# Performance work log

Measured on AMD Instinct MI355X. Metric: run time of the kernel, lower is better.

Reference implementation:

```python
import jax, jax.numpy as jnp
import numpy as np

N_NODE, N_USER, N_PRICE, EMB = 100000, 40000, 100, 128
E_VV, E_VP, E_VU, E_UV = 2000000, 200000, 2000000, 2000000


def _spmm(rows, cols, vals, x, n_rows):
    # sparse COO (n_rows, n_cols) @ x  -> (n_rows, d)
    return jax.ops.segment_sum(vals[:, None] * x[cols], rows, num_segments=n_rows)


def _row_norm_spmm(rows, cols, vals, x, n_rows):
    # torch.sparse.mm followed by division by row-sum of values (+1e-8)
    num = _spmm(rows, cols, vals, x, n_rows)
    den = jax.ops.segment_sum(vals, rows, num_segments=n_rows)[:, None] + 1e-8
    return num / den


def _linear(x, W, b):
    return x @ W.T + b


def setup_inputs() -> dict:
    key = jax.random.key(0)
    ks = jax.random.split(key, 40)
    d = {}
    d['embedding'] = jax.random.normal(ks[0], (N_NODE, EMB), jnp.float32) * 0.1
    d['pri_emb'] = jax.random.normal(ks[1], (N_PRICE, EMB), jnp.float32) * 0.1
    d['user_emb'] = jax.random.normal(ks[2], (N_USER, EMB), jnp.float32) * 0.1
    d['adj_rows'] = jax.random.randint(ks[3], (E_VV,), 0, N_NODE, jnp.int32)
    d['adj_cols'] = jax.random.randint(ks[4], (E_VV,), 0, N_NODE, jnp.int32)
    d['adj_vals'] = jax.random.uniform(ks[5], (E_VV,), jnp.float32)
    d['vp_rows'] = jax.random.randint(ks[6], (E_VP,), 0, N_NODE, jnp.int32)
    d['vp_cols'] = jax.random.randint(ks[7], (E_VP,), 0, N_PRICE, jnp.int32)
    d['vp_vals'] = jax.random.uniform(ks[8], (E_VP,), jnp.float32)
    d['vu_rows'] = jax.random.randint(ks[9], (E_VU,), 0, N_NODE, jnp.int32)
    d['vu_cols'] = jax.random.randint(ks[10], (E_VU,), 0, N_USER, jnp.int32)
    d['vu_vals'] = jax.random.uniform(ks[11], (E_VU,), jnp.float32)
    d['pv_rows'] = jax.random.randint(ks[12], (E_VP,), 0, N_PRICE, jnp.int32)
    d['pv_cols'] = jax.random.randint(ks[13], (E_VP,), 0, N_NODE, jnp.int32)
    d['pv_vals'] = jax.random.uniform(ks[14], (E_VP,), jnp.float32)
    d['uv_rows'] = jax.random.randint(ks[15], (E_UV,), 0, N_USER, jnp.int32)
    d['uv_cols'] = jax.random.randint(ks[16], (E_UV,), 0, N_NODE, jnp.int32)
    d['uv_vals'] = jax.random.uniform(ks[17], (E_UV,), jnp.float32)
    d['item_price_indices'] = jax.random.randint(ks[18], (N_NODE,), 0, N_PRICE, jnp.int32)
    s = 0.02
    d['mat_vu'] = jax.random.normal(ks[19], (N_NODE, 1), jnp.float32) * s
    d['mat_pv'] = jax.random.normal(ks[20], (N_PRICE, 1), jnp.float32) * s
    d['mat_uv'] = jax.random.normal(ks[21], (N_USER, 1), jnp.float32) * s
    d['W_aogi'] = jax.random.normal(ks[22], (EMB, 2 * EMB), jnp.float32) * s
    d['b_aogi'] = jnp.zeros((EMB,), jnp.float32)
    d['W_bgi1'] = jax.random.normal(ks[23], (EMB, EMB), jnp.float32) * s
    d['b_bgi1'] = jnp.zeros((EMB,), jnp.float32)
    d['W_aogp'] = jax.random.normal(ks[24], (EMB, 2 * EMB), jnp.float32) * s
    d['b_aogp'] = jnp.zeros((EMB,), jnp.float32)
    d['W_bgp1'] = jax.random.normal(ks[25], (EMB, EMB), jnp.float32) * s
    d['b_bgp1'] = jnp.zeros((EMB,), jnp.float32)
    d['W_user'] = jax.random.normal(ks[26], (EMB, 3 * EMB), jnp.float32) * s
    d['b_user'] = jnp.zeros((EMB,), jnp.float32)
    d['user_lambda'] = jnp.asarray(0.2, jnp.float32)
    return d


def _forward(embedding, pri_emb, user_emb,
             adj_rows, adj_cols, adj_vals,
             vp_rows, vp_cols, vp_vals,
             vu_rows, vu_cols, vu_vals,
             pv_rows, pv_cols, pv_vals,
             uv_rows, uv_cols, uv_vals,
             item_price_indices,
             mat_vu, mat_pv, mat_uv,
             W_aogi, b_aogi, W_bgi1, b_bgi1,
             W_aogp, b_aogp, W_bgp1, b_bgp1,
             W_user, b_user, user_lambda,
             layers=1):
    def inter_gate(Wa, ba, Wb, bb, e1, e2):
        gate = jax.nn.sigmoid(_linear(jnp.concatenate([e1, e2], 1), Wa, ba) + _linear(e1, Wb, bb))
        return e1 + gate * e2  # dropout50 = identity at eval

    def intra_gate(rows, cols, vals, mat_v, emb2, n_rows):
        # torch version computes the chunked row-normalized spmm under no_grad
        alpha = jax.lax.stop_gradient(_row_norm_spmm(rows, cols, vals, emb2, n_rows))
        return alpha * mat_v  # dropout70 = identity at eval

    for _ in range(layers):
        item = (inter_gate(W_aogi, b_aogi, W_bgi1, b_bgi1, embedding,
                           _spmm(vp_rows, vp_cols, vp_vals, pri_emb, N_NODE))
                + _spmm(adj_rows, adj_cols, adj_vals, embedding, N_NODE)
                + user_lambda * intra_gate(vu_rows, vu_cols, vu_vals, mat_vu, user_emb, N_NODE))
        price = inter_gate(W_aogp, b_aogp, W_bgp1, b_bgp1, pri_emb,
                           intra_gate(pv_rows, pv_cols, pv_vals, mat_pv, embedding, N_PRICE))
        e_price_user = _spmm(uv_rows, uv_cols, uv_vals, pri_emb[item_price_indices], N_USER)
        e_item_user = intra_gate(uv_rows, uv_cols, uv_vals, mat_uv, embedding, N_USER)
        gate = jax.nn.sigmoid(_linear(jnp.concatenate([user_emb, e_item_user, e_price_user], -1), W_user, b_user))
        user = gate * user_emb + (1.0 - gate) * e_item_user
        embedding, pri_emb, user_emb = item, price, user
    return item, price, user


def reference(embedding, pri_emb, user_emb,
              adj_rows, adj_cols, adj_vals,
              vp_rows, vp_cols, vp_vals,
              vu_rows, vu_cols, vu_vals,
              pv_rows, pv_cols, pv_vals,
              uv_rows, uv_cols, uv_vals,
              item_price_indices,
              mat_vu, mat_pv, mat_uv,
              W_aogi, b_aogi, W_bgi1, b_bgi1,
              W_aogp, b_aogp, W_bgp1, b_bgp1,
              W_user, b_user, user_lambda):
    return _forward(embedding, pri_emb, user_emb,
                    adj_rows, adj_cols, adj_vals,
                    vp_rows, vp_cols, vp_vals,
                    vu_rows, vu_cols, vu_vals,
                    pv_rows, pv_cols, pv_vals,
                    uv_rows, uv_cols, uv_vals,
                    item_price_indices,
                    mat_vu, mat_pv, mat_uv,
                    W_aogi, b_aogi, W_bgi1, b_bgi1,
                    W_aogp, b_aogp, W_bgp1, b_bgp1,
                    W_user, b_user, user_lambda)
```

## Files before the change

kernel.cpp:

```cpp
#include <hip/hip_runtime.h>
#include <hip/hip_bf16.h>

#define N_NODE 100000
#define N_USER 40000
#define N_PRICE 100
#define EMB 128
#define E_VV 2000000
#define E_VP 200000
#define E_VU 2000000
#define E_UV 2000000

#define FOFF0 0
#define FOFF1 256
#define FOFF2 512
#define FOFF3 767
#define FOFF4 1023
#define FTOT  1073
#define EPB   8192
#define BK1 245
#define BK2 490
#define BK3 735
#define BK4 760
#define BKT 785
#define CB1 256
#define CB2 512
#define CB3 767
#define CB4 1023
#define CBT 1073
#define RB_PV   100
#define RB_ITEM 25000
#define RB_USER 10000
#define RBT (RB_PV + RB_ITEM + RB_USER)
#define FB_ITEM 782
#define FB_USER 313
#define FBT (FB_ITEM + FB_USER + 50)

typedef __attribute__((ext_vector_type(8))) short short8;
typedef __attribute__((ext_vector_type(4))) float f32x4;

__device__ __forceinline__ float sigf(float x){ return 1.f/(1.f+__expf(-x)); }
__device__ __forceinline__ unsigned bfr(float f){
  unsigned u = __float_as_uint(f);
  return (u + 0x7FFFu + ((u>>16)&1u)) >> 16;
}
__device__ __forceinline__ float bf_lo(unsigned u){ return __uint_as_float(u << 16); }
__device__ __forceinline__ float bf_hi(unsigned u){ return __uint_as_float(u & 0xFFFF0000u); }
__device__ __forceinline__ unsigned pack2(float x, float y){ return bfr(x) | (bfr(y)<<16); }

__global__ __launch_bounds__(256) void k_cvt_all(
    const float4* __restrict__ se, const float4* __restrict__ su, const float4* __restrict__ sp,
    uint2* __restrict__ de, uint2* __restrict__ du, uint2* __restrict__ dp){
  const int nE = N_NODE*EMB/4, nU = N_USER*EMB/4, nP = N_PRICE*EMB/4;
  int i = blockIdx.x*256 + threadIdx.x;
  const float4* src; uint2* dst; int j;
  if (i < nE){ src = se; dst = de; j = i; }
  else if (i < nE+nU){ src = su; dst = du; j = i-nE; }
  else if (i < nE+nU+nP){ src = sp; dst = dp; j = i-nE-nU; }
  else return;
  float4 v = src[j];
  dst[j] = make_uint2(bfr(v.x) | (bfr(v.y)<<16), bfr(v.z) | (bfr(v.w)<<16));
}

__global__ __launch_bounds__(256) void k_prep(
    const float* __restrict__ Wa, const float* __restrict__ Wb, const float* __restrict__ Wu,
    ushort* __restrict__ Wc, ushort* __restrict__ Wub,
    int* __restrict__ fill,
    int2* __restrict__ adjE, int2* __restrict__ vuE, int2* __restrict__ uvE,
    int2* __restrict__ vpE, int2* __restrict__ pvE){
  if (blockIdx.x == 320){
    int t = threadIdx.x;
    for (int i = t; i < FTOT; i += 256) fill[i] = 0;
    if (t < 16){
      int2 z = make_int2(0,0);
      adjE[E_VV+t] = z; vuE[E_VU+t] = z; uvE[E_UV+t] = z; vpE[E_VP+t] = z; pvE[E_VP+t] = z;
    }
    return;
  }
  int idx = blockIdx.x*256 + threadIdx.x;
  if (idx < 128*256){
    int n = idx >> 8, k = idx & 255;
    float v = Wa[n*256+k] + ((k < 128) ? Wb[n*128+k] : 0.f);
    Wc[idx] = (ushort)bfr(v);
  } else {
    int j = idx - 128*256;
    if (j < 128*384) Wub[j] = (ushort)bfr(Wu[j]);
  }
}

template<int E, int RPB, int NB, int CAPc>
__device__ __forceinline__ void bucket_body(int blk,
    const int* __restrict__ rows, const int* __restrict__ cols, const float* __restrict__ vals,
    int* __restrict__ fill, uint2* __restrict__ stg,
    int* cnt, int* gbase, int* lbase, uint2* stage)
{
  const int t = threadIdx.x;
  const int e0 = blk * EPB;
  for (int i = t; i < NB; i += 256) cnt[i] = 0;
  __syncthreads();
  #pragma unroll 4
  for (int i = 0; i < 32; ++i){
    int e = e0 + i*256 + t;
    if (e < E) atomicAdd(&cnt[rows[e]/RPB], 1);
  }
  __syncthreads();
  if (t < 64){
    int run = 0;
    for (int c0 = 0; c0 < NB; c0 += 64){
      int j = c0 + t;
      int x = (j < NB) ? cnt[j] : 0;
      int s = x;
      #pragma unroll
      for (int d = 1; d < 64; d <<= 1){ int y = __shfl_up(s, d); if (t >= d) s += y; }
      if (j < NB) lbase[j] = run + s - x;
      run += __shfl(s, 63);
    }
  }
  __syncthreads();
  for (int b = t; b < NB; b += 256){
    int c = cnt[b];
    gbase[b] = (c > 0) ? atomicAdd(&fill[b], c) : 0;
    cnt[b] = lbase[b];
  }
  __syncthreads();
  #pragma unroll 4
  for (int i = 0; i < 32; ++i){
    int e = e0 + i*256 + t;
    if (e < E){
      int r = rows[e];
      int b = r/RPB, rl = r - b*RPB;
      int pos = atomicAdd(&cnt[b], 1);
      stage[pos] = make_uint2((unsigned)cols[e] | ((unsigned)rl << 17), __float_as_uint(vals[e]));
    }
  }
  __syncthreads();
  const int wid = t >> 6, lane = t & 63;
  for (int b = wid; b < NB; b += 4){
    int lb = lbase[b];
    int n = cnt[b] - lb;
    int gb = gbase[b];
    for (int j = lane; j < n; j += 64){
      int slot = gb + j; if (slot >= CAPc) slot = CAPc - 1;
      stg[(size_t)b*CAPc + slot] = stage[lb + j];
    }
  }
}

__global__ __launch_bounds__(256) void k_bucket_all(
    const int* __restrict__ aR, const int* __restrict__ aC, const float* __restrict__ aV,
    const int* __restrict__ uR, const int* __restrict__ uC, const float* __restrict__ uV,
    const int* __restrict__ vR, const int* __restrict__ vC, const float* __restrict__ vV,
    const int* __restrict__ pR, const int* __restrict__ pC, const float* __restrict__ pV,
    const int* __restrict__ qR, const int* __restrict__ qC, const float* __restrict__ qV,
    int* __restrict__ fill,
    uint2* __restrict__ stgA, uint2* __restrict__ stgU, uint2* __restrict__ stgV,
    uint2* __restrict__ stgP, uint2* __restrict__ stgQ)
{
  __shared__ int cnt[256], gbase[256], lbase[256];
  __shared__ uint2 stage[EPB];
  int b = blockIdx.x;
  if      (b < BK1) bucket_body<E_VV,391,256,8704>(b,      aR,aC,aV, fill+FOFF0, stgA, cnt, gbase, lbase, stage);
  else if (b < BK2) bucket_body<E_VU,391,256,8704>(b-BK1,  uR,uC,uV, fill+FOFF1, stgU, cnt, gbase, lbase, stage);
  else if (b < BK3) bucket_body<E_UV,157,255,8704>(b-BK2,  vR,vC,vV, fill+FOFF2, stgV, cnt, gbase, lbase, stage);
  else if (b < BK4) bucket_body<E_VP,391,256,1536>(b-BK3,  pR,pC,pV, fill+FOFF3, stgP, cnt, gbase, lbase, stage);
  else              bucket_body<E_VP,  2, 50,5120>(b-BK4,  qR,qC,qV, fill+FOFF4, stgQ, cnt, gbase, lbase, stage);
}

template<int NROW, int RPB, int NB, int CAPc>
__device__ __forceinline__ void csr_body(int b,
    const uint2* __restrict__ stg, const int* __restrict__ fill,
    int* __restrict__ start, int2* __restrict__ csr,
    int* cnt, uint2* stage, int* sbase)
{
  const int t = threadIdx.x;
  const int row0 = b * RPB;
  int R = NROW - row0; if (R > RPB) R = RPB;
  int count = fill[b]; if (count > CAPc) count = CAPc;
  for (int i = t; i < R; i += 256) cnt[i] = 0;
  if (t < 64){
    int run = 0;
    for (int c0 = 0; c0 < NB; c0 += 64){
      int j = c0 + t;
      int x = (j < NB) ? fill[j] : 0;
      int s = x;
      #pragma unroll
      for (int d = 1; d < 64; d <<= 1){ int y = __shfl_up(s, d); if (t >= d) s += y; }
      if (j == b) *sbase = run + s - x;
      run += __shfl(s, 63);
    }
  }
  __syncthreads();
  const int base = *sbase;
  const uint2* mystg = stg + (size_t)b*CAPc;
  for (int j = t; j < count; j += 256)
    atomicAdd(&cnt[mystg[j].x >> 17], 1);
  __syncthreads();
  if (t < 64){
    int run = 0;
    for (int c0 = 0; c0 < R; c0 += 64){
      int i = c0 + t;
      int x = (i < R) ? cnt[i] : 0;
      int s = x;
      #pragma unroll
      for (int d = 1; d < 64; d <<= 1){ int y = __shfl_up(s, d); if (t >= d) s += y; }
      if (i < R) cnt[i] = run + s - x;
      run += __shfl(s, 63);
    }
  }
  __syncthreads();
  for (int i = t; i < R; i += 256) start[row0 + i] = base + cnt[i];
  if (b == NB-1 && t == 0) start[NROW] = base + count;
  __syncthreads();
  for (int j = t; j < count; j += 256){
    uint2 kv = mystg[j];
    int rl = kv.x >> 17;
    int pos = atomicAdd(&cnt[rl], 1);
    stage[pos] = kv;
  }
  __syncthreads();
  for (int j = t; j < count; j += 256){
    uint2 kv = stage[j];
    csr[base + j] = make_int2((int)(kv.x & 0x1FFFF), (int)kv.y);
  }
}

__global__ __launch_bounds__(256) void k_csr_all(
    const uint2* __restrict__ stgA, const uint2* __restrict__ stgU, const uint2* __restrict__ stgV,
    const uint2* __restrict__ stgP, const uint2* __restrict__ stgQ,
    const int* __restrict__ fill,
    int* __restrict__ aS, int* __restrict__ uS, int* __restrict__ vS,
    int* __restrict__ pS, int* __restrict__ qS,
    int2* __restrict__ aE, int2* __restrict__ uE, int2* __restrict__ vE,
    int2* __restrict__ pE, int2* __restrict__ qE)
{
  __shared__ int cnt[391];
  __shared__ int sbase;
  __shared__ uint2 stage[8704];
  int b = blockIdx.x;
  if      (b < CB1) csr_body<N_NODE,391,256,8704>(b,     stgA, fill+FOFF0, aS, aE, cnt, stage, &sbase);
  else if (b < CB2) csr_body<N_NODE,391,256,8704>(b-CB1, stgU, fill+FOFF1, uS, uE, cnt, stage, &sbase);
  else if (b < CB3) csr_body<N_USER,157,255,8704>(b-CB2, stgV, fill+FOFF2, vS, vE, cnt, stage, &sbase);
  else if (b < CB4) csr_body<N_NODE,391,256,1536>(b-CB3, stgP, fill+FOFF3, pS, pE, cnt, stage, &sbase);
  else              csr_body<N_PRICE,  2, 50,5120>(b-CB4, stgQ, fill+FOFF4, qS, qE, cnt, stage, &sbase);
}


#define FMA8(ACC, U, V)                                     \
  ACC[0] += (V)*bf_lo((U).x); ACC[1] += (V)*bf_hi((U).x);   \
  ACC[2] += (V)*bf_lo((U).y); ACC[3] += (V)*bf_hi((U).y);   \
  ACC[4] += (V)*bf_lo((U).z); ACC[5] += (V)*bf_hi((U).z);   \
  ACC[6] += (V)*bf_lo((U).w); ACC[7] += (V)*bf_hi((U).w);

#define RED8(ACC)                                           \
  _Pragma("unroll")                                         \
  for (int j = 0; j < 8; ++j){                              \
    ACC[j] += __shfl_xor(ACC[j], 16);                       \
    ACC[j] += __shfl_xor(ACC[j], 32);                       \
  }

__device__ __forceinline__ void item_body(int rb,
    const uint4* __restrict__ be4, const uint4* __restrict__ bu4, const uint4* __restrict__ bp4,
    const int* __restrict__ aS, const int2* __restrict__ aE,
    const int* __restrict__ uS, const int2* __restrict__ uE,
    const int* __restrict__ pS, const int2* __restrict__ pE,
    const float* __restrict__ mat_vu, const float* __restrict__ lam,
    float4* __restrict__ out4, uint4* __restrict__ vp4)
{
  const int r = rb*4 + (threadIdx.x >> 6);
  const int l = threadIdx.x & 63;
  const int g = l >> 4, q = l & 15;
  float aA[8] = {}, aU[8] = {}, aP[8] = {};
  float den = 0.f;
  int s = aS[r], e = aS[r+1];
  for (int i = s; i < e; i += 16){
    int2 cv[4]; uint4 u[4];
    #pragma unroll
    for (int k = 0; k < 4; ++k) cv[k] = aE[i + 4*k + g];
    #pragma unroll
    for (int k = 0; k < 4; ++k) u[k] = be4[(size_t)cv[k].x*16 + q];
    #pragma unroll
    for (int k = 0; k < 4; ++k){
      float v = (i + 4*k + g < e) ? __int_as_float(cv[k].y) : 0.f;
      FMA8(aA, u[k], v)
    }
  }
  s = uS[r]; e = uS[r+1];
  for (int i = s; i < e; i += 16){
    int2 cv[4]; uint4 u[4];
    #pragma unroll
    for (int k = 0; k < 4; ++k) cv[k] = uE[i + 4*k + g];
    #pragma unroll
    for (int k = 0; k < 4; ++k) u[k] = bu4[(size_t)cv[k].x*16 + q];
    #pragma unroll
    for (int k = 0; k < 4; ++k){
      float v = (i + 4*k + g < e) ? __int_as_float(cv[k].y) : 0.f;
      FMA8(aU, u[k], v)
      den += v;
    }
  }
  s = pS[r]; e = pS[r+1];
  for (int i = s; i < e; i += 16){
    int2 cv[4]; uint4 u[4];
    #pragma unroll
    for (int k = 0; k < 4; ++k) cv[k] = pE[i + 4*k + g];
    #pragma unroll
    for (int k = 0; k < 4; ++k) u[k] = bp4[(size_t)cv[k].x*16 + q];
    #pragma unroll
    for (int k = 0; k < 4; ++k){
      float v = (i + 4*k + g < e) ? __int_as_float(cv[k].y) : 0.f;
      FMA8(aP, u[k], v)
    }
  }
  RED8(aA) RED8(aU) RED8(aP)
  den += __shfl_xor(den, 16); den += __shfl_xor(den, 32);
  float sc = lam[0]*mat_vu[r]/(den + 1e-8f);
  if (g == 0){
    out4[(size_t)r*32 + q*2]     = make_float4(aA[0]+sc*aU[0], aA[1]+sc*aU[1], aA[2]+sc*aU[2], aA[3]+sc*aU[3]);
    out4[(size_t)r*32 + q*2 + 1] = make_float4(aA[4]+sc*aU[4], aA[5]+sc*aU[5], aA[6]+sc*aU[6], aA[7]+sc*aU[7]);
    vp4[(size_t)r*16 + q] = make_uint4(pack2(aP[0],aP[1]), pack2(aP[2],aP[3]), pack2(aP[4],aP[5]), pack2(aP[6],aP[7]));
  }
}

__device__ __forceinline__ void user_body(int rb,
    const uint4* __restrict__ be4, const uint4* __restrict__ bp4,
    const int* __restrict__ S, const int2* __restrict__ E,
    const int* __restrict__ ipi, const float* __restrict__ mat_uv,
    uint4* __restrict__ eit4, uint4* __restrict__ uvp4)
{
  const int r = rb*4 + (threadIdx.x >> 6);
  const int l = threadIdx.x & 63;
  const int g = l >> 4, q = l & 15;
  float aI[8] = {}, aP[8] = {};
  float den = 0.f;
  int s = S[r], e = S[r+1];
  for (int i = s; i < e; i += 8){
    int2 cv[2];
    #pragma unroll
    for (int k = 0; k < 2; ++k) cv[k] = E[i + 4*k + g];
    uint4 u[2]; int ip[2];
    #pragma unroll
    for (int k = 0; k < 2; ++k){ u[k] = be4[(size_t)cv[k].x*16 + q]; ip[k] = ipi[cv[k].x]; }
    uint4 y[2];
    #pragma unroll
    for (int k = 0; k < 2; ++k) y[k] = bp4[(size_t)ip[k]*16 + q];
    #pragma unroll
    for (int k = 0; k < 2; ++k){
      float v = (i + 4*k + g < e) ? __int_as_float(cv[k].y) : 0.f;
      FMA8(aI, u[k], v)
      FMA8(aP, y[k], v)
      den += v;
    }
  }
  RED8(aI) RED8(aP)
  den += __shfl_xor(den, 16); den += __shfl_xor(den, 32);
  float sc = mat_uv[r]/(den + 1e-8f);
  if (g == 0){
    eit4[(size_t)r*16 + q] = make_uint4(pack2(sc*aI[0],sc*aI[1]), pack2(sc*aI[2],sc*aI[3]),
                                        pack2(sc*aI[4],sc*aI[5]), pack2(sc*aI[6],sc*aI[7]));
    uvp4[(size_t)r*16 + q] = make_uint4(pack2(aP[0],aP[1]), pack2(aP[2],aP[3]),
                                        pack2(aP[4],aP[5]), pack2(aP[6],aP[7]));
  }
}

__device__ __forceinline__ void pv_body(int r,
    const uint4* __restrict__ be4, const int2* __restrict__ E, const int* __restrict__ S,
    float* __restrict__ num, float* __restrict__ den_out)
{
  const int t = threadIdx.x;
  const int wid = t >> 6, l = t & 63;
  const int g = l >> 4, q = l & 15;
  float aP[8] = {}; float den = 0.f;
  int s = S[r], e = S[r+1];
  for (int i0 = s + wid*16; i0 < e; i0 += 64){
    int2 cv[4]; uint4 u[4];
    #pragma unroll
    for (int k = 0; k < 4; ++k) cv[k] = E[i0 + 4*k + g];
    #pragma unroll
    for (int k = 0; k < 4; ++k) u[k] = be4[(size_t)cv[k].x*16 + q];
    #pragma unroll
    for (int k = 0; k < 4; ++k){
      float v = (i0 + 4*k + g < e) ? __int_as_float(cv[k].y) : 0.f;
      FMA8(aP, u[k], v)
      den += v;
    }
  }
  RED8(aP)
  den += __shfl_xor(den, 16); den += __shfl_xor(den, 32);
  __shared__ float red[4][16][8];
  __shared__ float dred[4];
  if (g == 0){
    #pragma unroll
    for (int j = 0; j < 8; ++j) red[wid][q][j] = aP[j];
    if (l == 0) dred[wid] = den;
  }
  __syncthreads();
  if (t < 16){
    #pragma unroll
    for (int j = 0; j < 8; ++j)
      num[r*128 + t*8 + j] = red[0][t][j] + red[1][t][j] + red[2][t][j] + red[3][t][j];
    if (t == 0) den_out[r] = dred[0] + dred[1] + dred[2] + dred[3];
  }
}

__global__ __launch_bounds__(256) void k_rows_all(
    const uint4* __restrict__ be4, const uint4* __restrict__ bu4, const uint4* __restrict__ bp4,
    const int* __restrict__ aS, const int2* __restrict__ aE,
    const int* __restrict__ uS, const int2* __restrict__ uE,
    const int* __restrict__ pS, const int2* __restrict__ pE,
    const int* __restrict__ vS, const int2* __restrict__ vE,
    const int* __restrict__ qS, const int2* __restrict__ qE,
    const int* __restrict__ ipi,
    const float* __restrict__ mat_vu, const float* __restrict__ mat_uv, const float* __restrict__ lam,
    float4* __restrict__ out4, uint4* __restrict__ vp4,
    uint4* __restrict__ eit4, uint4* __restrict__ uvp4,
    float* __restrict__ pv_num, float* __restrict__ pv_den)
{
  int b = blockIdx.x;
  if (b < RB_PV){ pv_body(b, be4, qE, qS, pv_num, pv_den); return; }
  b -= RB_PV;
  if (b < RB_ITEM){ item_body(b, be4, bu4, bp4, aS, aE, uS, uE, pS, pE, mat_vu, lam, out4, vp4); return; }
  b -= RB_ITEM;
  user_body(b, be4, bp4, vS, vE, ipi, mat_uv, eit4, uvp4);
}

__device__ __forceinline__ void item_final_body(int blk, ushort* As, ushort* Bs,
    const ushort* __restrict__ A0, const ushort* __restrict__ A1,
    const ushort* __restrict__ W,
    const float* __restrict__ ba, const float* __restrict__ bb,
    float* __restrict__ out)
{
  const int t = threadIdx.x;
  const int l = t & 63, wv = t >> 6;
  const int wr = (wv>>1)*64, wc = (wv&1)*64;
  const int row0 = blk*128;
  const int lr16 = t >> 3;
  const int slot = t & 7;
  f32x4 acc[4][4] = {};
  for (int s = 0; s < 4; ++s){
    if (s) __syncthreads();
    const int k0 = s*64;
    const ushort* srcA = (k0 < 128) ? (A0 + k0) : (A1 + (k0 - 128));
    #pragma unroll
    for (int i = 0; i < 4; ++i){
      int r = i*32 + lr16;
      int gr = row0 + r; if (gr >= N_NODE) gr = N_NODE-1;
      uint4 va = *(const uint4*)(srcA + (size_t)gr*128 + slot*8);
      *(uint4*)&As[r*64 + ((slot*8) ^ ((r&7)*8))] = va;
      uint4 vb = *(const uint4*)(W + r*256 + k0 + slot*8);
      *(uint4*)&Bs[r*64 + ((slot*8) ^ ((r&7)*8))] = vb;
    }
    __syncthreads();
    #pragma unroll
    for (int kk = 0; kk < 64; kk += 32){
      short8 af[4], bf[4];
      #pragma unroll
      for (int f = 0; f < 4; ++f){
        int ar = wr + f*16 + (l&15);
        af[f] = *(const short8*)&As[ar*64 + ((kk + (l>>4)*8) ^ ((ar&7)*8))];
        int bn = wc + f*16 + (l&15);
        bf[f] = *(const short8*)&Bs[bn*64 + ((kk + (l>>4)*8) ^ ((bn&7)*8))];
      }
      #pragma unroll
      for (int fi = 0; fi < 4; ++fi)
        #pragma unroll
        for (int fj = 0; fj < 4; ++fj)
          acc[fi][fj] = __builtin_amdgcn_mfma_f32_16x16x32_bf16(af[fi], bf[fj], acc[fi][fj], 0, 0, 0);
    }
  }
  const int g4 = (l>>4)*4;
  #pragma unroll
  for (int fi = 0; fi < 4; ++fi){
    #pragma unroll
    for (int r = 0; r < 4; ++r){
      int grow = row0 + wr + fi*16 + g4 + r;
      if (grow < N_NODE){
        #pragma unroll
        for (int fj = 0; fj < 4; ++fj){
          int col = wc + fj*16 + (l&15);
          float x = acc[fi][fj][r] + ba[col] + bb[col];
          unsigned pv2 = *(const unsigned*)&A1[(size_t)grow*128 + (col & ~1)];
          float v = (col & 1) ? bf_hi(pv2) : bf_lo(pv2);
          unsigned em2 = *(const unsigned*)&A0[(size_t)grow*128 + (col & ~1)];
          float em = (col & 1) ? bf_hi(em2) : bf_lo(em2);
          size_t o = (size_t)grow*128 + col;
          out[o] = em + sigf(x)*v + out[o];
        }
      }
    }
  }
}

__device__ __forceinline__ void user_final_body(int blk, ushort* As, ushort* Bs,
    const ushort* __restrict__ A0, const ushort* __restrict__ A1, const ushort* __restrict__ A2,
    const ushort* __restrict__ W,
    const float* __restrict__ bu,
    float* __restrict__ out)
{
  const int t = threadIdx.x;
  const int l = t & 63, wv = t >> 6;
  const int wr = (wv>>1)*64, wc = (wv&1)*64;
  const int row0 = blk*128;
  const int lr16 = t >> 3;
  const int slot = t & 7;
  f32x4 acc[4][4] = {};
  for (int s = 0; s < 6; ++s){
    if (s) __syncthreads();
    const int k0 = s*64;
    const ushort* base = (s < 2) ? A0 : ((s < 4) ? A1 : A2);
    const ushort* srcA = base + (s & 1)*64;
    #pragma unroll
    for (int i = 0; i < 4; ++i){
      int r = i*32 + lr16;
      int gr = row0 + r; if (gr >= N_USER) gr = N_USER-1;
      uint4 va = *(const uint4*)(srcA + (size_t)gr*128 + slot*8);
      *(uint4*)&As[r*64 + ((slot*8) ^ ((r&7)*8))] = va;
      uint4 vb = *(const uint4*)(W + r*384 + k0 + slot*8);
      *(uint4*)&Bs[r*64 + ((slot*8) ^ ((r&7)*8))] = vb;
    }
    __syncthreads();
    #pragma unroll
    for (int kk = 0; kk < 64; kk += 32){
      short8 af[4], bf[4];
      #pragma unroll
      for (int f = 0; f < 4; ++f){
        int ar = wr + f*16 + (l&15);
        af[f] = *(const short8*)&As[ar*64 + ((kk + (l>>4)*8) ^ ((ar&7)*8))];
        int bn = wc + f*16 + (l&15);
        bf[f] = *(const short8*)&Bs[bn*64 + ((kk + (l>>4)*8) ^ ((bn&7)*8))];
      }
      #pragma unroll
      for (int fi = 0; fi < 4; ++fi)
        #pragma unroll
        for (int fj = 0; fj < 4; ++fj)
          acc[fi][fj] = __builtin_amdgcn_mfma_f32_16x16x32_bf16(af[fi], bf[fj], acc[fi][fj], 0, 0, 0);
    }
  }
  const int g4 = (l>>4)*4;
  #pragma unroll
  for (int fi = 0; fi < 4; ++fi){
    #pragma unroll
    for (int r = 0; r < 4; ++r){
      int grow = row0 + wr + fi*16 + g4 + r;
      if (grow < N_USER){
        #pragma unroll
        for (int fj = 0; fj < 4; ++fj){
          int col = wc + fj*16 + (l&15);
          float g = sigf(acc[fi][fj][r] + bu[col]);
          unsigned e2 = *(const unsigned*)&A1[(size_t)grow*128 + (col & ~1)];
          float ei = (col & 1) ? bf_hi(e2) : bf_lo(e2);
          unsigned u2 = *(const unsigned*)&A0[(size_t)grow*128 + (col & ~1)];
          float uu = (col & 1) ? bf_hi(u2) : bf_lo(u2);
          size_t o = (size_t)grow*128 + col;
          out[o] = g*uu + (1.f - g)*ei;
        }
      }
    }
  }
}

__device__ __forceinline__ void price_final_body(int blk, float* A2,
    const float* __restrict__ pe, const float* __restrict__ num, const float* __restrict__ den,
    const float* __restrict__ mat_pv,
    const float* __restrict__ Wa, const float* __restrict__ ba,
    const float* __restrict__ Wb, const float* __restrict__ bb,
    float* __restrict__ out_price)
{
  int t = threadIdx.x;
  #pragma unroll
  for (int i = 0; i < 2; ++i){
    int flat = i*256 + t;
    int rl = flat >> 8; int k = flat & 255;
    int r = blk*2 + rl;
    float v;
    if (k < 128) v = pe[r*128 + k];
    else         v = num[r*128 + (k-128)] / (den[r] + 1e-8f) * mat_pv[r];
    A2[rl*256 + k] = v;
  }
  __syncthreads();
  int rl = t >> 7; int c = t & 127;
  int r = blk*2 + rl;
  float x = 0.f;
  #pragma unroll 4
  for (int k = 0; k < 256; ++k){
    float w = (k < 128) ? (Wa[c*256 + k] + Wb[c*128 + k]) : Wa[c*256 + k];
    x += A2[rl*256 + k]*w;
  }
  float g = sigf(x + ba[c] + bb[c]);
  out_price[r*128 + c] = pe[r*128 + c] + g*A2[rl*256 + 128 + c];
}

__global__ __launch_bounds__(256) void k_finals_all(
    const ushort* __restrict__ bemb, const ushort* __restrict__ vp_bf, const ushort* __restrict__ Wc,
    const float* __restrict__ b_aogi, const float* __restrict__ b_bgi1,
    float* __restrict__ out_item,
    const ushort* __restrict__ bue, const ushort* __restrict__ eitem_bf, const ushort* __restrict__ uvp_bf,
    const ushort* __restrict__ Wub, const float* __restrict__ b_user,
    float* __restrict__ out_user,
    const float* __restrict__ pe, const float* __restrict__ pv_num, const float* __restrict__ pv_den,
    const float* __restrict__ mat_pv,
    const float* __restrict__ W_aogp, const float* __restrict__ b_aogp,
    const float* __restrict__ W_bgp1, const float* __restrict__ b_bgp1,
    float* __restrict__ out_price)
{
  __shared__ __align__(16) ushort As[128*64];
  __shared__ __align__(16) ushort Bs[128*64];
  __shared__ float A2[512];
  int b = blockIdx.x;
  if (b < FB_ITEM){
    item_final_body(b, As, Bs, bemb, vp_bf, Wc, b_aogi, b_bgi1, out_item);
  } else if (b < FB_ITEM + FB_USER){
    user_final_body(b - FB_ITEM, As, Bs, bue, eitem_bf, uvp_bf, Wub, b_user, out_user);
  } else {
    price_final_body(b - FB_ITEM - FB_USER, A2, pe, pv_num, pv_den, mat_pv,
                     W_aogp, b_aogp, W_bgp1, b_bgp1, out_price);
  }
}

extern "C" void kernel_launch(void* const* d_in, const int* in_sizes, int n_in,
                              void* d_out, int out_size, void* d_ws, size_t ws_size,
                              hipStream_t stream){
  (void)in_sizes; (void)n_in; (void)out_size; (void)ws_size;
  const float* emb = (const float*)d_in[0];
  const float* pe  = (const float*)d_in[1];
  const float* ue  = (const float*)d_in[2];
  const int*   adj_r = (const int*)d_in[3];  const int* adj_c = (const int*)d_in[4];  const float* adj_v = (const float*)d_in[5];
  const int*   vp_r  = (const int*)d_in[6];  const int* vp_c  = (const int*)d_in[7];  const float* vp_v  = (const float*)d_in[8];
  const int*   vu_r  = (const int*)d_in[9];  const int* vu_c  = (const int*)d_in[10]; const float* vu_v  = (const float*)d_in[11];
  const int*   pv_r  = (const int*)d_in[12]; const int* pv_c  = (const int*)d_in[13]; const float* pv_v  = (const float*)d_in[14];
  const int*   uv_r  = (const int*)d_in[15]; const int* uv_c  = (const int*)d_in[16]; const float* uv_v  = (const float*)d_in[17];
  const int*   ipi   = (const int*)d_in[18];
  const float* mat_vu = (const float*)d_in[19];
  const float* mat_pv = (const float*)d_in[20];
  const float* mat_uv = (const float*)d_in[21];
  const float* W_aogi = (const float*)d_in[22]; const float* b_aogi = (const float*)d_in[23];
  const float* W_bgi1 = (const float*)d_in[24]; const float* b_bgi1 = (const float*)d_in[25];
  const float* W_aogp = (const float*)d_in[26]; const float* b_aogp = (const float*)d_in[27];
  const float* W_bgp1 = (const float*)d_in[28]; const float* b_bgp1 = (const float*)d_in[29];
  const float* W_user = (const float*)d_in[30]; const float* b_user = (const float*)d_in[31];
  const float* lam    = (const float*)d_in[32];

  float* out_item  = (float*)d_out;
  float* out_price = out_item + (size_t)N_NODE*EMB;
  float* out_user  = out_price + (size_t)N_PRICE*EMB;

  char* w = (char*)d_ws;
  size_t off = 0;
  auto alloc = [&](size_t bytes)->char*{
    char* p = w + off;
    off = (off + bytes + 255) & ~(size_t)255;
    return p;
  };
  int* fill = (int*)alloc(FTOT*4);
  int* aS  = (int*)alloc((N_NODE+1)*4);
  int* uS  = (int*)alloc((N_NODE+1)*4);
  int* vS  = (int*)alloc((N_USER+1)*4);
  int* pS  = (int*)alloc((N_NODE+1)*4);
  int* qS  = (int*)alloc(101*4);
  ushort* Wc_item = (ushort*)alloc(128*256*2);
  ushort* Wu_bf   = (ushort*)alloc(128*384*2);
  char* region = alloc((size_t)93*1024*1024);
  uint2* stgA = (uint2*)region;
  uint2* stgU = (uint2*)(region + (size_t)256*8704*8);
  uint2* stgV = (uint2*)(region + (size_t)2*256*8704*8);
  uint2* stgP = (uint2*)(region + (size_t)3*256*8704*8);
  uint2* stgQ = (uint2*)(region + (size_t)3*256*8704*8 + (size_t)256*1536*8);
  unsigned* bemb = (unsigned*)region;
  unsigned* bue  = (unsigned*)(region + (size_t)N_NODE*EMB*2);
  unsigned* bpe  = (unsigned*)(region + (size_t)(N_NODE+N_USER)*EMB*2);
  unsigned* vp_bf = (unsigned*)(region + (size_t)37*1024*1024);
  int2*  adjE = (int2*)alloc(((size_t)E_VV+16)*8);
  int2*  vuE  = (int2*)alloc(((size_t)E_VU+16)*8);
  int2*  uvE  = (int2*)alloc(((size_t)E_UV+16)*8);
  int2*  vpE  = (int2*)alloc(((size_t)E_VP+16)*8);
  int2*  pvE  = (int2*)alloc(((size_t)E_VP+16)*8);
  unsigned* eitem_bf = (unsigned*)alloc((size_t)N_USER*64*4);
  unsigned* uvp_bf   = (unsigned*)alloc((size_t)N_USER*64*4);
  float* pv_num   = (float*)alloc((size_t)N_PRICE*EMB*4);
  float* pv_den   = (float*)alloc(N_PRICE*4);

  k_prep<<<321,256,0,stream>>>(W_aogi, W_bgi1, W_user, Wc_item, Wu_bf,
                               fill, adjE, vuE, uvE, vpE, pvE);

  k_bucket_all<<<BKT,256,0,stream>>>(
      adj_r,adj_c,adj_v, vu_r,vu_c,vu_v, uv_r,uv_c,uv_v, vp_r,vp_c,vp_v, pv_r,pv_c,pv_v,
      fill, stgA, stgU, stgV, stgP, stgQ);

  k_csr_all<<<CBT,256,0,stream>>>(stgA, stgU, stgV, stgP, stgQ, fill,
      aS, uS, vS, pS, qS, adjE, vuE, uvE, vpE, pvE);

  k_cvt_all<<<((N_NODE+N_USER+N_PRICE)*EMB/4+255)/256,256,0,stream>>>(
      (const float4*)emb, (const float4*)ue, (const float4*)pe,
      (uint2*)bemb, (uint2*)bue, (uint2*)bpe);

  k_rows_all<<<RBT,256,0,stream>>>(
      (const uint4*)bemb, (const uint4*)bue, (const uint4*)bpe,
      aS, adjE, uS, vuE, pS, vpE, vS, uvE, qS, pvE,
      ipi, mat_vu, mat_uv, lam,
      (float4*)out_item, (uint4*)vp_bf, (uint4*)eitem_bf, (uint4*)uvp_bf,
      pv_num, pv_den);

  k_finals_all<<<FBT,256,0,stream>>>(
      (const ushort*)bemb, (const ushort*)vp_bf, Wc_item, b_aogi, b_bgi1, out_item,
      (const ushort*)bue, (const ushort*)eitem_bf, (const ushort*)uvp_bf, Wu_bf, b_user, out_user,
      pe, pv_num, pv_den, mat_pv, W_aogp, b_aogp, W_bgp1, b_bgp1, out_price);
}
```

Before: 543.1 us.

## Fuse prep, bucketing and bf16 conversion into one front kernel; stage buckets in output buffer

Result: faster. 511.1 us (-5.9%).

```diff
diff --git a/kernel.cpp b/kernel.cpp
--- a/kernel.cpp
+++ b/kernel.cpp
@@ -22,6 +22,9 @@
 #define BK3 735
 #define BK4 760
 #define BKT 785
+#define NCVT 17513
+#define FR_CVT (BKT + NCVT)
+#define FR_TOT (FR_CVT + 320)
 #define CB1 256
 #define CB2 512
 #define CB3 767
@@ -47,46 +50,6 @@
 __device__ __forceinline__ float bf_hi(unsigned u){ return __uint_as_float(u & 0xFFFF0000u); }
 __device__ __forceinline__ unsigned pack2(float x, float y){ return bfr(x) | (bfr(y)<<16); }
 
-__global__ __launch_bounds__(256) void k_cvt_all(
-    const float4* __restrict__ se, const float4* __restrict__ su, const float4* __restrict__ sp,
-    uint2* __restrict__ de, uint2* __restrict__ du, uint2* __restrict__ dp){
-  const int nE = N_NODE*EMB/4, nU = N_USER*EMB/4, nP = N_PRICE*EMB/4;
-  int i = blockIdx.x*256 + threadIdx.x;
-  const float4* src; uint2* dst; int j;
-  if (i < nE){ src = se; dst = de; j = i; }
-  else if (i < nE+nU){ src = su; dst = du; j = i-nE; }
-  else if (i < nE+nU+nP){ src = sp; dst = dp; j = i-nE-nU; }
-  else return;
-  float4 v = src[j];
-  dst[j] = make_uint2(bfr(v.x) | (bfr(v.y)<<16), bfr(v.z) | (bfr(v.w)<<16));
-}
-
-__global__ __launch_bounds__(256) void k_prep(
-    const float* __restrict__ Wa, const float* __restrict__ Wb, const float* __restrict__ Wu,
-    ushort* __restrict__ Wc, ushort* __restrict__ Wub,
-    int* __restrict__ fill,
-    int2* __restrict__ adjE, int2* __restrict__ vuE, int2* __restrict__ uvE,
-    int2* __restrict__ vpE, int2* __restrict__ pvE){
-  if (blockIdx.x == 320){
-    int t = threadIdx.x;
-    for (int i = t; i < FTOT; i += 256) fill[i] = 0;
-    if (t < 16){
-      int2 z = make_int2(0,0);
-      adjE[E_VV+t] = z; vuE[E_VU+t] = z; uvE[E_UV+t] = z; vpE[E_VP+t] = z; pvE[E_VP+t] = z;
-    }
-    return;
-  }
-  int idx = blockIdx.x*256 + threadIdx.x;
-  if (idx < 128*256){
-    int n = idx >> 8, k = idx & 255;
-    float v = Wa[n*256+k] + ((k < 128) ? Wb[n*128+k] : 0.f);
-    Wc[idx] = (ushort)bfr(v);
-  } else {
-    int j = idx - 128*256;
-    if (j < 128*384) Wub[j] = (ushort)bfr(Wu[j]);
-  }
-}
-
 template<int E, int RPB, int NB, int CAPc>
 __device__ __forceinline__ void bucket_body(int blk,
     const int* __restrict__ rows, const int* __restrict__ cols, const float* __restrict__ vals,
@@ -145,7 +108,7 @@
   }
 }
 
-__global__ __launch_bounds__(256) void k_bucket_all(
+__global__ __launch_bounds__(256) void k_front(
     const int* __restrict__ aR, const int* __restrict__ aC, const float* __restrict__ aV,
     const int* __restrict__ uR, const int* __restrict__ uC, const float* __restrict__ uV,
     const int* __restrict__ vR, const int* __restrict__ vC, const float* __restrict__ vV,
@@ -153,16 +116,44 @@
     const int* __restrict__ qR, const int* __restrict__ qC, const float* __restrict__ qV,
     int* __restrict__ fill,
     uint2* __restrict__ stgA, uint2* __restrict__ stgU, uint2* __restrict__ stgV,
-    uint2* __restrict__ stgP, uint2* __restrict__ stgQ)
+    uint2* __restrict__ stgP, uint2* __restrict__ stgQ,
+    const float4* __restrict__ se, const float4* __restrict__ su, const float4* __restrict__ sp,
+    uint2* __restrict__ de, uint2* __restrict__ du, uint2* __restrict__ dp,
+    const float* __restrict__ Wa, const float* __restrict__ Wb, const float* __restrict__ Wu,
+    ushort* __restrict__ Wc, ushort* __restrict__ Wub)
 {
   __shared__ int cnt[256], gbase[256], lbase[256];
   __shared__ uint2 stage[EPB];
   int b = blockIdx.x;
-  if      (b < BK1) bucket_body<E_VV,391,256,8704>(b,      aR,aC,aV, fill+FOFF0, stgA, cnt, gbase, lbase, stage);
-  else if (b < BK2) bucket_body<E_VU,391,256,8704>(b-BK1,  uR,uC,uV, fill+FOFF1, stgU, cnt, gbase, lbase, stage);
-  else if (b < BK3) bucket_body<E_UV,157,255,8704>(b-BK2,  vR,vC,vV, fill+FOFF2, stgV, cnt, gbase, lbase, stage);
-  else if (b < BK4) bucket_body<E_VP,391,256,1536>(b-BK3,  pR,pC,pV, fill+FOFF3, stgP, cnt, gbase, lbase, stage);
-  else              bucket_body<E_VP,  2, 50,5120>(b-BK4,  qR,qC,qV, fill+FOFF4, stgQ, cnt, gbase, lbase, stage);
+  if (b < BKT){
+    if      (b < BK1) bucket_body<E_VV,391,256,8704>(b,      aR,aC,aV, fill+FOFF0, stgA, cnt, gbase, lbase, stage);
+    else if (b < BK2) bucket_body<E_VU,391,256,8704>(b-BK1,  uR,uC,uV, fill+FOFF1, stgU, cnt, gbase, lbase, stage);
+    else if (b < BK3) bucket_body<E_UV,157,255,8704>(b-BK2,  vR,vC,vV, fill+FOFF2, stgV, cnt, gbase, lbase, stage);
+    else if (b < BK4) bucket_body<E_VP,391,256,1536>(b-BK3,  pR,pC,pV, fill+FOFF3, stgP, cnt, gbase, lbase, stage);
+    else              bucket_body<E_VP,  2, 50,5120>(b-BK4,  qR,qC,qV, fill+FOFF4, stgQ, cnt, gbase, lbase, stage);
+    return;
+  }
+  if (b < FR_CVT){
+    const int nE = N_NODE*EMB/4, nU = N_USER*EMB/4, nP = N_PRICE*EMB/4;
+    int i = (b - BKT)*256 + threadIdx.x;
+    const float4* src; uint2* dst; int j;
+    if (i < nE){ src = se; dst = de; j = i; }
+    else if (i < nE+nU){ src = su; dst = du; j = i-nE; }
+    else if (i < nE+nU+nP){ src = sp; dst = dp; j = i-nE-nU; }
+    else return;
+    float4 v = src[j];
+    dst[j] = make_uint2(bfr(v.x) | (bfr(v.y)<<16), bfr(v.z) | (bfr(v.w)<<16));
+    return;
+  }
+  int idx = (b - FR_CVT)*256 + threadIdx.x;
+  if (idx < 128*256){
+    int n = idx >> 8, k = idx & 255;
+    float v = Wa[n*256+k] + ((k < 128) ? Wb[n*128+k] : 0.f);
+    Wc[idx] = (ushort)bfr(v);
+  } else {
+    int j = idx - 128*256;
+    if (j < 128*384) Wub[j] = (ushort)bfr(Wu[j]);
+  }
 }
 
 template<int NROW, int RPB, int NB, int CAPc>
@@ -276,7 +267,7 @@
     #pragma unroll
     for (int k = 0; k < 4; ++k) cv[k] = aE[i + 4*k + g];
     #pragma unroll
-    for (int k = 0; k < 4; ++k) u[k] = be4[(size_t)cv[k].x*16 + q];
+    for (int k = 0; k < 4; ++k) u[k] = be4[(size_t)(cv[k].x & 0x1FFFF)*16 + q];
     #pragma unroll
     for (int k = 0; k < 4; ++k){
       float v = (i + 4*k + g < e) ? __int_as_float(cv[k].y) : 0.f;
@@ -289,7 +280,7 @@
     #pragma unroll
     for (int k = 0; k < 4; ++k) cv[k] = uE[i + 4*k + g];
     #pragma unroll
-    for (int k = 0; k < 4; ++k) u[k] = bu4[(size_t)cv[k].x*16 + q];
+    for (int k = 0; k < 4; ++k) u[k] = bu4[(size_t)(cv[k].x & 0x1FFFF)*16 + q];
     #pragma unroll
     for (int k = 0; k < 4; ++k){
       float v = (i + 4*k + g < e) ? __int_as_float(cv[k].y) : 0.f;
@@ -303,7 +294,7 @@
     #pragma unroll
     for (int k = 0; k < 4; ++k) cv[k] = pE[i + 4*k + g];
     #pragma unroll
-    for (int k = 0; k < 4; ++k) u[k] = bp4[(size_t)cv[k].x*16 + q];
+    for (int k = 0; k < 4; ++k) u[k] = bp4[(size_t)(cv[k].x & 0x1FFFF)*16 + q];
     #pragma unroll
     for (int k = 0; k < 4; ++k){
       float v = (i + 4*k + g < e) ? __int_as_float(cv[k].y) : 0.f;
@@ -338,7 +329,11 @@
     for (int k = 0; k < 2; ++k) cv[k] = E[i + 4*k + g];
     uint4 u[2]; int ip[2];
     #pragma unroll
-    for (int k = 0; k < 2; ++k){ u[k] = be4[(size_t)cv[k].x*16 + q]; ip[k] = ipi[cv[k].x]; }
+    for (int k = 0; k < 2; ++k){
+      int c = cv[k].x & 0x1FFFF;
+      u[k] = be4[(size_t)c*16 + q];
+      ip[k] = ipi[c < N_NODE ? c : N_NODE-1];
+    }
     uint4 y[2];
     #pragma unroll
     for (int k = 0; k < 2; ++k) y[k] = bp4[(size_t)ip[k]*16 + q];
@@ -375,7 +370,7 @@
     #pragma unroll
     for (int k = 0; k < 4; ++k) cv[k] = E[i0 + 4*k + g];
     #pragma unroll
-    for (int k = 0; k < 4; ++k) u[k] = be4[(size_t)cv[k].x*16 + q];
+    for (int k = 0; k < 4; ++k) u[k] = be4[(size_t)(cv[k].x & 0x1FFFF)*16 + q];
     #pragma unroll
     for (int k = 0; k < 4; ++k){
       float v = (i0 + 4*k + g < e) ? __int_as_float(cv[k].y) : 0.f;
@@ -642,6 +637,14 @@
   float* out_price = out_item + (size_t)N_NODE*EMB;
   float* out_user  = out_price + (size_t)N_PRICE*EMB;
 
+  char* ob = (char*)d_out;
+  const size_t SEGBIG = (size_t)256*8704*8;
+  uint2* stgA = (uint2*)ob;
+  uint2* stgU = (uint2*)(ob + SEGBIG);
+  uint2* stgV = (uint2*)(ob + 2*SEGBIG);
+  uint2* stgP = (uint2*)(ob + 3*SEGBIG);
+  uint2* stgQ = (uint2*)(ob + 3*SEGBIG + (size_t)256*1536*8);
+
   char* w = (char*)d_ws;
   size_t off = 0;
   auto alloc = [&](size_t bytes)->char*{
@@ -657,16 +660,11 @@
   int* qS  = (int*)alloc(101*4);
   ushort* Wc_item = (ushort*)alloc(128*256*2);
   ushort* Wu_bf   = (ushort*)alloc(128*384*2);
-  char* region = alloc((size_t)93*1024*1024);
-  uint2* stgA = (uint2*)region;
-  uint2* stgU = (uint2*)(region + (size_t)256*8704*8);
-  uint2* stgV = (uint2*)(region + (size_t)2*256*8704*8);
-  uint2* stgP = (uint2*)(region + (size_t)3*256*8704*8);
-  uint2* stgQ = (uint2*)(region + (size_t)3*256*8704*8 + (size_t)256*1536*8);
+  char* region = alloc((size_t)62*1024*1024);
   unsigned* bemb = (unsigned*)region;
   unsigned* bue  = (unsigned*)(region + (size_t)N_NODE*EMB*2);
   unsigned* bpe  = (unsigned*)(region + (size_t)(N_NODE+N_USER)*EMB*2);
-  unsigned* vp_bf = (unsigned*)(region + (size_t)37*1024*1024);
+  unsigned* vp_bf = (unsigned*)(region + (size_t)(N_NODE+N_USER+N_PRICE)*EMB*2);
   int2*  adjE = (int2*)alloc(((size_t)E_VV+16)*8);
   int2*  vuE  = (int2*)alloc(((size_t)E_VU+16)*8);
   int2*  uvE  = (int2*)alloc(((size_t)E_UV+16)*8);
@@ -677,19 +675,17 @@
   float* pv_num   = (float*)alloc((size_t)N_PRICE*EMB*4);
   float* pv_den   = (float*)alloc(N_PRICE*4);
 
-  k_prep<<<321,256,0,stream>>>(W_aogi, W_bgi1, W_user, Wc_item, Wu_bf,
-                               fill, adjE, vuE, uvE, vpE, pvE);
-
-  k_bucket_all<<<BKT,256,0,stream>>>(
+  hipMemsetAsync(fill, 0, FTOT*4, stream);
+
+  k_front<<<FR_TOT,256,0,stream>>>(
       adj_r,adj_c,adj_v, vu_r,vu_c,vu_v, uv_r,uv_c,uv_v, vp_r,vp_c,vp_v, pv_r,pv_c,pv_v,
-      fill, stgA, stgU, stgV, stgP, stgQ);
+      fill, stgA, stgU, stgV, stgP, stgQ,
+      (const float4*)emb, (const float4*)ue, (const float4*)pe,
+      (uint2*)bemb, (uint2*)bue, (uint2*)bpe,
+      W_aogi, W_bgi1, W_user, Wc_item, Wu_bf);
 
   k_csr_all<<<CBT,256,0,stream>>>(stgA, stgU, stgV, stgP, stgQ, fill,
       aS, uS, vS, pS, qS, adjE, vuE, uvE, vpE, pvE);
-
-  k_cvt_all<<<((N_NODE+N_USER+N_PRICE)*EMB/4+255)/256,256,0,stream>>>(
-      (const float4*)emb, (const float4*)ue, (const float4*)pe,
-      (uint2*)bemb, (uint2*)bue, (uint2*)bpe);
 
   k_rows_all<<<RBT,256,0,stream>>>(
       (const uint4*)bemb, (const uint4*)bue, (const uint4*)bpe,
```
